# Kernel optimization log

Hardware: AMD Instinct MI355X
Metric: run time of the kernel (lower is better)

## Reference

```python
import jax, jax.numpy as jnp
import numpy as np

C = 1.0            # curvature
MIN_NORM = 1e-15   # hgcn min_norm
PROJ_EPS = 4e-3    # hgcn PoincareBall float32 boundary eps
N, D, E = 100000, 128, 1600000


def _artanh(x):
    # hgcn Artanh clamps input away from +-1 for stability
    return jnp.arctanh(jnp.clip(x, -1.0 + 1e-5, 1.0 - 1e-5))


def logmap0(p, c):
    sqrt_c = c ** 0.5
    p_norm = jnp.maximum(jnp.linalg.norm(p, axis=-1, keepdims=True), MIN_NORM)
    return p * _artanh(sqrt_c * p_norm) / (sqrt_c * p_norm)


def expmap0(u, c):
    sqrt_c = c ** 0.5
    u_norm = jnp.maximum(jnp.linalg.norm(u, axis=-1, keepdims=True), MIN_NORM)
    return jnp.tanh(sqrt_c * u_norm) * u / (sqrt_c * u_norm)


def proj(x, c):
    norm = jnp.maximum(jnp.linalg.norm(x, axis=-1, keepdims=True), MIN_NORM)
    maxnorm = (1.0 - PROJ_EPS) / (c ** 0.5)
    return jnp.where(norm > maxnorm, x / norm * maxnorm, x)


def setup_inputs() -> dict:
    key = jax.random.key(0)
    k1, k2, k3, k4 = jax.random.split(key, 4)
    # node features on the Poincare ball (small tangent vectors -> exp -> proj)
    x = proj(0.05 * jax.random.normal(k1, (N, D), dtype=jnp.float32), C)
    rows = jax.random.randint(k2, (E,), 0, N, dtype=jnp.int32)   # dst nodes
    cols = jax.random.randint(k3, (E,), 0, N, dtype=jnp.int32)   # src nodes
    # positive edge weights, roughly row-normalized (avg degree 16)
    vals = jax.random.uniform(k4, (E,), dtype=jnp.float32) / 16.0
    return {"x": x, "rows": rows, "cols": cols, "vals": vals}


def reference(x, rows, cols, vals):
    # x_tangent = logmap0(x)
    x_tangent = logmap0(x, C)                         # [N, D]
    # support_t = spmm(adj, x_tangent): gather src features, weight, scatter-add to dst
    msgs = vals[:, None] * x_tangent[cols]            # [E, D]
    support_t = jax.ops.segment_sum(msgs, rows, num_segments=N)  # [N, D]
    # output = proj(expmap0(support_t))
    return proj(expmap0(support_t, C), C)
```

## Files before the change

kernel.cpp:

```cpp
#include <hip/hip_runtime.h>
#include <hip/hip_fp16.h>
#include <math.h>

#define DIM 128
#define MAXNORM (1.0f - 4e-3f)
#define RPB 64
#define EPB 4096
#define CAP 48
#define CSTRIDE 32
#define RBLK 512
#define GTHREADS 256
#define FCAP 64

__device__ __forceinline__ float wave_reduce_sum(float v) {
    #pragma unroll
    for (int off = 32; off > 0; off >>= 1)
        v += __shfl_xor(v, off, 64);
    return v;
}

__device__ __forceinline__ unsigned pack_h2(float a, float b) {
    unsigned lo = (unsigned)__half_as_ushort(__float2half_rn(a));
    unsigned hi = (unsigned)__half_as_ushort(__float2half_rn(b));
    return lo | (hi << 16);
}

__device__ __forceinline__ float tanh_fast(float x) {
    float e = __expf(2.0f * x);
    return 1.0f - 2.0f / (e + 1.0f);
}

__global__ void xt_kernel(const float* __restrict__ x,
                          unsigned* __restrict__ xt, int n,
                          int* __restrict__ bcur, int nb) {
    if (bcur != nullptr) {
        int nzb = (gridDim.x < 8u) ? (int)gridDim.x : 8;
        if ((int)blockIdx.x < nzb) {
            for (int i = (int)blockIdx.x * 256 + (int)threadIdx.x; i < nb; i += nzb * 256)
                bcur[i] = 0;
        }
    }
    int wave = (int)((blockIdx.x * blockDim.x + threadIdx.x) >> 6);
    int lane = threadIdx.x & 63;
    if (wave >= n) return;
    const float2* xr = (const float2*)(x + (size_t)wave * DIM);
    float2 v = xr[lane];
    float ss = wave_reduce_sum(v.x * v.x + v.y * v.y);
    float norm = sqrtf(ss);
    float t = fminf(norm, 1.0f - 1e-5f);
    float at = 0.5f * logf((1.0f + t) / (1.0f - t));
    float f = at / fmaxf(norm, 1e-15f);
    xt[(size_t)wave * 64 + lane] = pack_h2(v.x * f, v.y * f);
}

__global__ void reorder_kernel(const int* __restrict__ rows, const int* __restrict__ cols,
                               const float* __restrict__ vals,
                               int* __restrict__ bcur,
                               float* __restrict__ out, int E, int NB, int CAPB) {
    extern __shared__ int locCur[];
    int tid = threadIdx.x;
    int base = blockIdx.x * EPB;

    int er[8]; int ec[8]; float ev[8];
    #pragma unroll
    for (int k = 0; k < 8; k++) {
        int e = base + k * RBLK + tid;
        bool ok = e < E;
        er[k] = ok ? rows[e] : -1;
        ec[k] = ok ? cols[e] : 0;
        ev[k] = ok ? vals[e] : 0.f;
    }

    for (int i = tid; i < NB; i += RBLK) locCur[i] = 0;
    __syncthreads();
    #pragma unroll
    for (int k = 0; k < 8; k++)
        if (er[k] >= 0) atomicAdd(&locCur[er[k] >> 6], 1);
    __syncthreads();
    for (int i = tid; i < NB; i += RBLK) {
        int a = locCur[i];
        locCur[i] = a ? atomicAdd(&bcur[i], a) : 0;
    }
    __syncthreads();
    #pragma unroll
    for (int k = 0; k < 8; k++) {
        if (er[k] >= 0) {
            int r = er[k];
            int b = r >> 6, lr = r & (RPB - 1);
            unsigned hw = (unsigned)__half_as_ushort(__float2half(ev[k])) & 0x7fffu;
            unsigned rx = (hw << 17) | (unsigned)ec[k];
            int slot = atomicAdd(&locCur[b], 1);
            if (slot < CAPB) {
                uint2* recs = (uint2*)((char*)out + ((size_t)b << 15));
                recs[slot] = make_uint2(rx, (unsigned)lr);
            }
        }
    }
}

__global__ void __launch_bounds__(GTHREADS, 4)
bucket_gather_kernel(const unsigned* __restrict__ xt,
                     const int* __restrict__ bcur,
                     float* __restrict__ out, int n, int CAPB) {
    __shared__ unsigned ell[RPB * CAP];
    __shared__ int cnt[RPB];
    int b = blockIdx.x;
    int tid = threadIdx.x;
    int row0 = b * RPB;
    int rowsInB = n - row0; if (rowsInB > RPB) rowsInB = RPB;
    for (int i = tid; i < RPB; i += GTHREADS) cnt[i] = 0;
    __syncthreads();
    int total = bcur[b]; if (total > CAPB) total = CAPB;
    const uint2* recs = (const uint2*)((const char*)out + ((size_t)b << 15));
    for (int i = tid; i < total; i += GTHREADS) {
        uint2 rec = recs[i];
        int lr = (int)rec.y;
        int p = atomicAdd(&cnt[lr], 1);
        if (p < CAP) ell[lr * CAP + p] = rec.x;
    }
    __syncthreads();
    if (tid < RPB) {
        int d = cnt[tid]; if (d > CAP) d = CAP;
        int dp = (d + 7) & ~7; if (dp > CAP) dp = CAP;
        for (int q = d; q < dp; ++q) ell[tid * CAP + q] = 0;
    }
    __syncthreads();
    int wv = tid >> 6, lane = tid & 63;
    unsigned lane4 = (unsigned)(lane << 2);
    for (int lr = wv; lr < rowsInB; lr += GTHREADS / 64) {
        int deg = cnt[lr]; if (deg > CAP) deg = CAP;
        float ax = 0.f, ay = 0.f;
        const unsigned* erow = &ell[lr * CAP];
        for (int j = 0; j < deg; j += 8) {
            uint4 qa = *(const uint4*)(erow + j);
            uint4 qb = *(const uint4*)(erow + j + 4);
            unsigned pk[8] = {qa.x, qa.y, qa.z, qa.w, qb.x, qb.y, qb.z, qb.w};
            __half2 u[8];
            #pragma unroll
            for (int k = 0; k < 8; k++) {
                unsigned voff = ((pk[k] & 0x1ffffu) << 8) + lane4;
                u[k] = *(const __half2*)((const char*)xt + voff);
            }
            #pragma unroll
            for (int k = 0; k < 8; k++) {
                float w = __half2float(__ushort_as_half((unsigned short)(pk[k] >> 17)));
                ax = fmaf(w, __low2float(u[k]), ax);
                ay = fmaf(w, __high2float(u[k]), ay);
            }
        }
        float ssum = wave_reduce_sum(ax * ax + ay * ay);
        float n0 = fmaxf(sqrtf(ssum), 1e-15f);
        float th = tanh_fast(n0);
        float f = (th > MAXNORM) ? (MAXNORM / n0) : (th / n0);
        float2* o = (float2*)(out + (size_t)(row0 + lr) * DIM);
        o[lane] = make_float2(ax * f, ay * f);
    }
}

__global__ void scatter_ell_kernel(const int* __restrict__ rows,
                                   const int* __restrict__ cols,
                                   const float* __restrict__ vals,
                                   int* __restrict__ cur,
                                   unsigned* __restrict__ ell, int E) {
    int e = blockIdx.x * blockDim.x + threadIdx.x;
    if (e >= E) return;
    int r = rows[e];
    unsigned hb = (unsigned)__half_as_ushort(__float2half(vals[e])) & 0x7fffu;
    unsigned pk = ((unsigned)cols[e] << 15) | hb;
    int pos = atomicAdd(&cur[(size_t)r * CSTRIDE], 1);
    if (pos < FCAP) ell[(size_t)r * FCAP + pos] = pk;
}

__global__ void gather_ell_kernel(const unsigned* __restrict__ xt,
                                  const unsigned* __restrict__ ell,
                                  const int* __restrict__ cur,
                                  float* __restrict__ out, int n) {
    int wave = (int)((blockIdx.x * blockDim.x + threadIdx.x) >> 6);
    int lane = threadIdx.x & 63;
    if (wave >= n) return;
    const __half2* xt2 = (const __half2*)xt;
    int deg = cur[(size_t)wave * CSTRIDE];
    if (deg > FCAP) deg = FCAP;
    unsigned pl = 0;
    if (lane < deg) pl = ell[(size_t)wave * FCAP + lane];
    float2 acc = make_float2(0.f, 0.f);
    for (int j = 0; j < deg; j += 8) {
        float w[8]; __half2 u[8]; int c[8];
        #pragma unroll
        for (int k = 0; k < 8; k++) {
            int idx = j + k;
            bool ok = idx < deg;
            unsigned p = __shfl(pl, ok ? idx : 0);
            c[k] = (int)(p >> 15);
            w[k] = ok ? __half2float(__ushort_as_half((unsigned short)(p & 0x7fffu))) : 0.f;
        }
        #pragma unroll
        for (int k = 0; k < 8; k++)
            u[k] = xt2[(size_t)c[k] * 64 + lane];
        #pragma unroll
        for (int k = 0; k < 8; k++) {
            acc.x = fmaf(w[k], __low2float(u[k]), acc.x);
            acc.y = fmaf(w[k], __high2float(u[k]), acc.y);
        }
    }
    float ss = wave_reduce_sum(acc.x * acc.x + acc.y * acc.y);
    float n0 = fmaxf(sqrtf(ss), 1e-15f);
    float th = tanhf(n0);
    float f = (th > MAXNORM) ? (MAXNORM / n0) : (th / n0);
    float2* o = (float2*)(out + (size_t)wave * DIM);
    o[lane] = make_float2(acc.x * f, acc.y * f);
}

__global__ void tangent_kernel(const float* __restrict__ x,
                               float* __restrict__ xt, int n) {
    int wave = (int)((blockIdx.x * blockDim.x + threadIdx.x) >> 6);
    int lane = threadIdx.x & 63;
    if (wave >= n) return;
    const float2* xr = (const float2*)(x + (size_t)wave * DIM);
    float2 v = xr[lane];
    float ss = wave_reduce_sum(v.x * v.x + v.y * v.y);
    float norm = sqrtf(ss);
    float t = fminf(norm, 1.0f - 1e-5f);
    float at = 0.5f * logf((1.0f + t) / (1.0f - t));
    float factor = at / fmaxf(norm, 1e-15f);
    float2* o = (float2*)(xt + (size_t)wave * DIM);
    o[lane] = make_float2(v.x * factor, v.y * factor);
}

__global__ void scatter_kernel(const float* __restrict__ xt,
                               const int* __restrict__ rows,
                               const int* __restrict__ cols,
                               const float* __restrict__ vals,
                               float* __restrict__ out, int E) {
    long gid = (long)blockIdx.x * blockDim.x + threadIdx.x;
    int e = (int)(gid >> 5);
    int lane = (int)(gid & 31);
    if (e >= E) return;
    int r = rows[e];
    int c = cols[e];
    float w = vals[e];
    const float4* src = (const float4*)(xt + (size_t)c * DIM);
    float4 v = src[lane];
    float* dst = out + (size_t)r * DIM + lane * 4;
    unsafeAtomicAdd(dst + 0, v.x * w);
    unsafeAtomicAdd(dst + 1, v.y * w);
    unsafeAtomicAdd(dst + 2, v.z * w);
    unsafeAtomicAdd(dst + 3, v.w * w);
}

__global__ void finalize_kernel(float* __restrict__ out, int n) {
    int wave = (int)((blockIdx.x * blockDim.x + threadIdx.x) >> 6);
    int lane = threadIdx.x & 63;
    if (wave >= n) return;
    float2* p = (float2*)(out + (size_t)wave * DIM);
    float2 v = p[lane];
    float ss = wave_reduce_sum(v.x * v.x + v.y * v.y);
    float n0 = fmaxf(sqrtf(ss), 1e-15f);
    float th = tanhf(n0);
    float factor = (th > MAXNORM) ? (MAXNORM / n0) : (th / n0);
    p[lane] = make_float2(v.x * factor, v.y * factor);
}

extern "C" void kernel_launch(void* const* d_in, const int* in_sizes, int n_in,
                              void* d_out, int out_size, void* d_ws, size_t ws_size,
                              hipStream_t stream) {
    const float* x    = (const float*)d_in[0];
    const int*   rows = (const int*)d_in[1];
    const int*   cols = (const int*)d_in[2];
    const float* vals = (const float*)d_in[3];
    float* out = (float*)d_out;

    int n = in_sizes[0] / DIM;
    int E = in_sizes[1];
    int NB = (n + RPB - 1) / RPB;

    auto align256 = [](size_t b) { return (b + 255) & ~(size_t)255; };

    size_t xt_b = align256((size_t)n * 64 * 4);
    size_t nb_b = align256((size_t)NB * 4);
    size_t reorder_lds = (size_t)NB * 4;

    double mean = (n > 0) ? (double)E * RPB / (double)n : 0.0;
    int req = (int)(mean + 8.0 * sqrt(mean + 1.0)) + 32;
    int capb = (req + 31) & ~31;
    int tail = n - (NB - 1) * RPB;

    if (n > 0 && n <= (1 << 17) && capb <= 4000 &&
        (size_t)capb * 8 <= (size_t)tail * 512 &&
        reorder_lds <= 60 * 1024 && xt_b + nb_b <= ws_size) {
        unsigned* xt_h = (unsigned*)d_ws;
        int*      bcur = (int*)((char*)d_ws + xt_b);

        xt_kernel<<<(n + 3) / 4, 256, 0, stream>>>(x, xt_h, n, bcur, NB);
        if (E > 0) {
            int NEB = (E + EPB - 1) / EPB;
            reorder_kernel<<<NEB, RBLK, reorder_lds, stream>>>(rows, cols, vals,
                                                               bcur, out, E, NB, capb);
        }
        bucket_gather_kernel<<<NB, GTHREADS, 0, stream>>>(xt_h, bcur, out, n, capb);
        return;
    }

    size_t ell_b = align256((size_t)n * FCAP * 4);
    size_t cur_b = align256((size_t)n * CSTRIDE * 4);
    if (n <= (1 << 17) && xt_b + ell_b + cur_b <= ws_size) {
        unsigned* xt_h = (unsigned*)d_ws;
        unsigned* ell  = (unsigned*)((char*)d_ws + xt_b);
        int*      cur  = (int*)((char*)d_ws + xt_b + ell_b);
        xt_kernel<<<(n + 3) / 4, 256, 0, stream>>>(x, xt_h, n, nullptr, 0);
        hipMemsetAsync(cur, 0, (size_t)n * CSTRIDE * 4, stream);
        scatter_ell_kernel<<<(E + 255) / 256, 256, 0, stream>>>(rows, cols, vals, cur, ell, E);
        gather_ell_kernel<<<(n + 3) / 4, 256, 0, stream>>>(xt_h, ell, cur, out, n);
        return;
    }

    float* xtf = (float*)d_in[0];
    size_t xtb = (size_t)n * DIM * sizeof(float);
    if (ws_size >= xtb) xtf = (float*)d_ws;
    tangent_kernel<<<(n + 3) / 4, 256, 0, stream>>>(x, xtf, n);
    hipMemsetAsync(d_out, 0, (size_t)n * DIM * sizeof(float), stream);
    long threads = (long)E * 32;
    scatter_kernel<<<(int)((threads + 255) / 256), 256, 0, stream>>>(xtf, rows, cols, vals, out, E);
    finalize_kernel<<<(n + 3) / 4, 256, 0, stream>>>(out, n);
}
```

Measured before the change: 214.0 us.

## Split edge bucketing into two-level radix partition via super-buckets

Replaces the single-pass reorder, which scattered edge records straight into 1563 per-64-row buckets with global atomics, with two passes. The first pass partitions edges into coarser super-buckets of 512 rows in workspace. The second pass splits each super-bucket into its 8 fine buckets using shared-memory counters and writes the final per-bucket counts. The aim is to shrink the global atomic contention and LDS histogram size and to make the scatter writes more coalesced. The cost is an extra kernel launch, an extra read and write of all edge records, and a larger workspace requirement.

```diff
diff --git a/kernel.cpp b/kernel.cpp
--- a/kernel.cpp
+++ b/kernel.cpp
@@ -5,6 +5,8 @@
 #define DIM 128
 #define MAXNORM (1.0f - 4e-3f)
 #define RPB 64
+#define SUPF 8
+#define SUPR (RPB * SUPF)
 #define EPB 4096
 #define CAP 48
 #define CSTRIDE 32
@@ -32,12 +34,12 @@
 
 __global__ void xt_kernel(const float* __restrict__ x,
                           unsigned* __restrict__ xt, int n,
-                          int* __restrict__ bcur, int nb) {
-    if (bcur != nullptr) {
+                          int* __restrict__ zbuf, int nz) {
+    if (zbuf != nullptr) {
         int nzb = (gridDim.x < 8u) ? (int)gridDim.x : 8;
         if ((int)blockIdx.x < nzb) {
-            for (int i = (int)blockIdx.x * 256 + (int)threadIdx.x; i < nb; i += nzb * 256)
-                bcur[i] = 0;
+            for (int i = (int)blockIdx.x * 256 + (int)threadIdx.x; i < nz; i += nzb * 256)
+                zbuf[i] = 0;
         }
     }
     int wave = (int)((blockIdx.x * blockDim.x + threadIdx.x) >> 6);
@@ -53,10 +55,10 @@
     xt[(size_t)wave * 64 + lane] = pack_h2(v.x * f, v.y * f);
 }
 
-__global__ void reorder_kernel(const int* __restrict__ rows, const int* __restrict__ cols,
-                               const float* __restrict__ vals,
-                               int* __restrict__ bcur,
-                               float* __restrict__ out, int E, int NB, int CAPB) {
+__global__ void partA_kernel(const int* __restrict__ rows, const int* __restrict__ cols,
+                             const float* __restrict__ vals,
+                             int* __restrict__ scur, uint2* __restrict__ sup,
+                             int E, int NSB, int CAPS) {
     extern __shared__ int locCur[];
     int tid = threadIdx.x;
     int base = blockIdx.x * EPB;
@@ -71,30 +73,56 @@
         ev[k] = ok ? vals[e] : 0.f;
     }
 
-    for (int i = tid; i < NB; i += RBLK) locCur[i] = 0;
+    for (int i = tid; i < NSB; i += RBLK) locCur[i] = 0;
     __syncthreads();
     #pragma unroll
     for (int k = 0; k < 8; k++)
-        if (er[k] >= 0) atomicAdd(&locCur[er[k] >> 6], 1);
-    __syncthreads();
-    for (int i = tid; i < NB; i += RBLK) {
+        if (er[k] >= 0) atomicAdd(&locCur[er[k] >> 9], 1);
+    __syncthreads();
+    for (int i = tid; i < NSB; i += RBLK) {
         int a = locCur[i];
-        locCur[i] = a ? atomicAdd(&bcur[i], a) : 0;
+        locCur[i] = a ? atomicAdd(&scur[i], a) : 0;
     }
     __syncthreads();
     #pragma unroll
     for (int k = 0; k < 8; k++) {
         if (er[k] >= 0) {
             int r = er[k];
-            int b = r >> 6, lr = r & (RPB - 1);
+            int s = r >> 9;
             unsigned hw = (unsigned)__half_as_ushort(__float2half(ev[k])) & 0x7fffu;
             unsigned rx = (hw << 17) | (unsigned)ec[k];
-            int slot = atomicAdd(&locCur[b], 1);
-            if (slot < CAPB) {
-                uint2* recs = (uint2*)((char*)out + ((size_t)b << 15));
-                recs[slot] = make_uint2(rx, (unsigned)lr);
-            }
-        }
+            int slot = atomicAdd(&locCur[s], 1);
+            if (slot < CAPS)
+                sup[(size_t)s * CAPS + slot] = make_uint2(rx, (unsigned)r);
+        }
+    }
+}
+
+__global__ void partB_kernel(const int* __restrict__ scur, const uint2* __restrict__ sup,
+                             int* __restrict__ bcur, float* __restrict__ out,
+                             int NB, int CAPS, int CAPB) {
+    __shared__ int cur[SUPF];
+    int s = blockIdx.x;
+    int tid = threadIdx.x;
+    if (tid < SUPF) cur[tid] = 0;
+    __syncthreads();
+    int total = scur[s]; if (total > CAPS) total = CAPS;
+    const uint2* src = sup + (size_t)s * CAPS;
+    for (int i = tid; i < total; i += blockDim.x) {
+        uint2 rec = src[i];
+        unsigned r = rec.y;
+        int b = (int)(r >> 6);
+        int f = b & (SUPF - 1);
+        int slot = atomicAdd(&cur[f], 1);
+        if (slot < CAPB) {
+            uint2* recs = (uint2*)((char*)out + ((size_t)b << 15));
+            recs[slot] = make_uint2(rec.x, r & (RPB - 1));
+        }
+    }
+    __syncthreads();
+    if (tid < SUPF) {
+        int b = s * SUPF + tid;
+        if (b < NB) bcur[b] = (cur[tid] < CAPB) ? cur[tid] : CAPB;
     }
 }
 
@@ -272,30 +300,38 @@
 
     int n = in_sizes[0] / DIM;
     int E = in_sizes[1];
-    int NB = (n + RPB - 1) / RPB;
+    int NB  = (n + RPB - 1) / RPB;
+    int NSB = (n + SUPR - 1) / SUPR;
 
     auto align256 = [](size_t b) { return (b + 255) & ~(size_t)255; };
 
     size_t xt_b = align256((size_t)n * 64 * 4);
-    size_t nb_b = align256((size_t)NB * 4);
-    size_t reorder_lds = (size_t)NB * 4;
-
-    double mean = (n > 0) ? (double)E * RPB / (double)n : 0.0;
-    int req = (int)(mean + 8.0 * sqrt(mean + 1.0)) + 32;
-    int capb = (req + 31) & ~31;
+
+    double fmean = (n > 0) ? (double)E * RPB / (double)n : 0.0;
+    int capb = ((int)(fmean + 8.0 * sqrt(fmean + 1.0)) + 63) & ~63;
+    double smean = (NSB > 0) ? (double)E / (double)NSB : 0.0;
+    int caps = ((int)(smean + 8.0 * sqrt(smean + 1.0)) + 127) & ~127;
     int tail = n - (NB - 1) * RPB;
+
+    size_t sup_b  = align256((size_t)NSB * (size_t)caps * 8);
+    size_t meta_b = align256((size_t)(NSB + NB) * 4);
+    size_t need   = xt_b + sup_b + meta_b;
+    size_t partA_lds = (size_t)NSB * 4;
 
     if (n > 0 && n <= (1 << 17) && capb <= 4000 &&
         (size_t)capb * 8 <= (size_t)tail * 512 &&
-        reorder_lds <= 60 * 1024 && xt_b + nb_b <= ws_size) {
+        partA_lds <= 60 * 1024 && need <= ws_size) {
         unsigned* xt_h = (unsigned*)d_ws;
-        int*      bcur = (int*)((char*)d_ws + xt_b);
-
-        xt_kernel<<<(n + 3) / 4, 256, 0, stream>>>(x, xt_h, n, bcur, NB);
+        uint2*    sup  = (uint2*)((char*)d_ws + xt_b);
+        int*      scur = (int*)((char*)d_ws + xt_b + sup_b);
+        int*      bcur = scur + NSB;
+
+        xt_kernel<<<(n + 3) / 4, 256, 0, stream>>>(x, xt_h, n, scur, NSB + NB);
         if (E > 0) {
             int NEB = (E + EPB - 1) / EPB;
-            reorder_kernel<<<NEB, RBLK, reorder_lds, stream>>>(rows, cols, vals,
-                                                               bcur, out, E, NB, capb);
+            partA_kernel<<<NEB, RBLK, partA_lds, stream>>>(rows, cols, vals,
+                                                           scur, sup, E, NSB, caps);
+            partB_kernel<<<NSB, RBLK, 0, stream>>>(scur, sup, bcur, out, NB, caps, capb);
         }
         bucket_gather_kernel<<<NB, GTHREADS, 0, stream>>>(xt_h, bcur, out, n, capb);
         return;
```

Measured after the change: 215.9 us. No clear change (+0.9%).
